# Kernel tuning notes

Measured on AMD Instinct MI355X. Metric: run time of the kernel, lower is better.

## Reference

```python
import jax, jax.numpy as jnp
import numpy as np

B, C, H, W, T_PREV, HEADS, KSIZE = 16, 512, 28, 28, 15, 16, 5


def setup_inputs() -> dict:
    key = jax.random.key(0)
    ks = jax.random.split(key, 6)
    return {
        "x": jax.random.normal(ks[0], (B, C, H, W), jnp.float32),
        "prev_K": jax.random.normal(ks[1], (B, T_PREV, C), jnp.float32),
        "prev_V": jax.random.normal(ks[2], (B, T_PREV, C, H, W), jnp.float32) * 0.1,
        "wq": jax.random.normal(ks[3], (1, 1, KSIZE), jnp.float32) * 0.3,
        "wk": jax.random.normal(ks[4], (1, 1, KSIZE), jnp.float32) * 0.3,
        "wv": jax.random.normal(ks[5], (C, 1, 3, 3), jnp.float32) * 0.2,
    }


def _conv1d_same(y, ker):
    # y: [b,1,c], ker: [1,1,k]; SAME padding = (k-1)//2 on each side for odd k
    p = (ker.shape[-1] - 1) // 2
    return jax.lax.conv_general_dilated(
        y, ker, (1,), [(p, p)], dimension_numbers=("NCH", "OIH", "NCH"))


def _forward(x, prev_K, prev_V, wq, wk, wv):
    b, c, h, w = x.shape
    g = HEADS
    d = c // g
    norm = 1.0 / jnp.sqrt(jnp.asarray(d, x.dtype))
    # ECA-style channel attention: global avg pool -> conv1d over channels
    y = jnp.mean(x, axis=(2, 3))[:, None, :]            # [b,1,c]
    Q = _conv1d_same(y, wq)[:, 0, :]                    # [b,c]
    k = _conv1d_same(y, wk)                             # [b,1,c]
    # depthwise 3x3 conv for V
    v = jax.lax.conv_general_dilated(
        x, wv, (1, 1), [(1, 1), (1, 1)],
        dimension_numbers=("NCHW", "OIHW", "NCHW"), feature_group_count=c)
    # grow recurrent caches
    K = jnp.concatenate([prev_K, k], axis=1)            # [b,t,c]
    V = jnp.concatenate([prev_V, v[:, None]], axis=1)   # [b,t,c,h,w]
    t = K.shape[1]
    # grouped decode attention: single query step vs t cached steps
    Qg = Q.reshape(b, g, d)                             # [b,g,d]
    Kg = K.reshape(b, t, g, d)                          # [b,t,g,d]
    atten = jnp.einsum("bgd,btgd->bgt", Qg, Kg) * norm  # [b,g,t]
    atten = jax.nn.softmax(atten, axis=-1)
    Vg = V.reshape(b, t, g, d, h, w)                    # [b,t,g,d,h,w]
    out = jnp.einsum("bgt,btgdhw->bgdhw", atten, Vg).reshape(b, c, h, w)
    return out, K, V


def reference(x, prev_K, prev_V, wq, wk, wv):
    return _forward(x, prev_K, prev_V, wq, wk, wv)
```

## Files before the change

### kernel.cpp

```cpp
#include <hip/hip_runtime.h>
#include <hip/hip_bf16.h>

#define B_ 16
#define C_ 512
#define H_ 28
#define W_ 28
#define TPREV 15
#define TT 16
#define HEADS_ 16
#define DHEAD 32
#define HW 784
#define HW4 196
#define CH4 (C_ * HW4)
#define NORM 0.17677669529663687f

typedef float f32x4 __attribute__((ext_vector_type(4)));

#define POOL_BLOCKS (B_ * C_)
#define KCOPY_QUADS (B_ * TPREV * C_ / 4)
#define KCOPY_BLOCKS (KCOPY_QUADS / 64)

__global__ __launch_bounds__(64) void pool_copy_kernel(const float* __restrict__ x,
                                                       const float* __restrict__ prevK,
                                                       float* __restrict__ y,
                                                       float* __restrict__ Kout) {
    const int lane = threadIdx.x;
    if (blockIdx.x < POOL_BLOCKS) {
        const int bc = blockIdx.x;
        const f32x4* __restrict__ xr = (const f32x4*)(x + (size_t)bc * HW);
        float s = 0.0f;
        for (int i = lane; i < HW4; i += 64) {
            f32x4 v = xr[i];
            s += v.x + v.y + v.z + v.w;
        }
        #pragma unroll
        for (int off = 32; off > 0; off >>= 1) s += __shfl_down(s, off);
        if (lane == 0) y[bc] = s * (1.0f / (float)HW);
    } else {
        const int j = (blockIdx.x - POOL_BLOCKS) * 64 + lane;
        const f32x4* __restrict__ src = (const f32x4*)prevK;
        f32x4* __restrict__ dst = (f32x4*)Kout;
        const int b = j / (TPREV * C_ / 4);
        dst[j + b * (C_ / 4)] = src[j];
    }
}

__global__ __launch_bounds__(256) void fuse_kernel(const float* __restrict__ x,
                                                   const float* __restrict__ prevV,
                                                   const float* __restrict__ prevK,
                                                   const float* __restrict__ y,
                                                   const float* __restrict__ wq,
                                                   const float* __restrict__ wk,
                                                   const float* __restrict__ wv,
                                                   float* __restrict__ out,
                                                   float* __restrict__ Kout,
                                                   float* __restrict__ Vout) {
    const int tid = threadIdx.x;
    const int blk0 = blockIdx.x * 256;
    __shared__ float att_s[3][TT];

    const int bc_lo = blk0 / HW4;
    const int bc_hi = (blk0 + 255) / HW4;

    if (tid < 96) {
        const int half = tid >> 5;
        const int d    = tid & 31;
        const int bcx  = bc_lo + half;
        if (bcx <= bc_hi) {
            const int bb = bcx >> 9;
            const int gg = (bcx & (C_ - 1)) >> 5;
            const int cc = gg * DHEAD + d;

            float Qc = 0.0f, kc = 0.0f;
            #pragma unroll
            for (int j = 0; j < 5; ++j) {
                const int cj = cc - 2 + j;
                const float yv = (cj >= 0 && cj < C_) ? y[bb * C_ + cj] : 0.0f;
                Qc = fmaf(yv, wq[j], Qc);
                kc = fmaf(yv, wk[j], kc);
            }

            float pl[TT];
            #pragma unroll
            for (int t = 0; t < TPREV; ++t)
                pl[t] = Qc * prevK[((size_t)bb * TPREV + t) * C_ + cc];
            pl[TPREV] = Qc * kc;

            #pragma unroll
            for (int m = 1; m <= 16; m <<= 1) {
                #pragma unroll
                for (int t = 0; t < TT; ++t)
                    pl[t] += __shfl_xor(pl[t], m);
            }

            float mx = -1e30f;
            #pragma unroll
            for (int t = 0; t < TT; ++t) mx = fmaxf(mx, pl[t] * NORM);
            float sum = 0.0f;
            #pragma unroll
            for (int t = 0; t < TT; ++t) sum += __expf(pl[t] * NORM - mx);
            if (d < TT)
                att_s[half][d] = __expf(pl[d] * NORM - mx) / sum;

            const int qk = (bb * C_ + cc) * HW4;
            if (qk >= blk0 && qk < blk0 + 256)
                Kout[((size_t)bb * TT + TPREV) * C_ + cc] = kc;
        }
    }
    __syncthreads();

    const int i  = blk0 + tid;
    const int p4 = i % HW4;
    const int bc = i / HW4;
    const int c  = bc & (C_ - 1);
    const int b  = bc >> 9;
    const int h_ = bc - bc_lo;

    f32x4* __restrict__ Vo = (f32x4*)Vout;
    const f32x4* __restrict__ Pv = (const f32x4*)prevV;
    const size_t pvq = ((size_t)b * TPREV * C_ + c) * HW4 + p4;
    const size_t voq = ((size_t)b * TT    * C_ + c) * HW4 + p4;

    f32x4 pv[TPREV];
    #pragma unroll
    for (int t = 0; t < TPREV; ++t)
        pv[t] = __builtin_nontemporal_load(&Pv[pvq + (size_t)t * CH4]);

    const float* __restrict__ xbc = x + (size_t)bc * HW;
    const int p  = p4 * 4;
    const int h  = p / W_;
    const int w0 = p % W_;
    float r[3][6];
    #pragma unroll
    for (int ry = 0; ry < 3; ++ry) {
        const int hh = h - 1 + ry;
        if (hh < 0 || hh >= H_) {
            #pragma unroll
            for (int j = 0; j < 6; ++j) r[ry][j] = 0.0f;
        } else {
            const float* row = xbc + hh * W_;
            f32x4 mid = *(const f32x4*)(row + w0);
            r[ry][1] = mid.x; r[ry][2] = mid.y; r[ry][3] = mid.z; r[ry][4] = mid.w;
            r[ry][0] = (w0 > 0)      ? row[w0 - 1] : 0.0f;
            r[ry][5] = (w0 + 4 < W_) ? row[w0 + 4] : 0.0f;
        }
    }
    float wv9[9];
    #pragma unroll
    for (int k = 0; k < 9; ++k) wv9[k] = wv[c * 9 + k];

    f32x4 v4;
    #pragma unroll
    for (int j = 0; j < 4; ++j) {
        float s = 0.0f;
        #pragma unroll
        for (int ky = 0; ky < 3; ++ky)
            #pragma unroll
            for (int kx = 0; kx < 3; ++kx)
                s = fmaf(r[ky][j + kx], wv9[ky * 3 + kx], s);
        v4[j] = s;
    }

    f32x4 acc;
    {
        const float a = att_s[h_][TPREV];
        __builtin_nontemporal_store(v4, &Vo[voq + (size_t)TPREV * CH4]);
        acc = v4 * a;
    }

    #pragma unroll
    for (int t = 0; t < TPREV; ++t) {
        __builtin_nontemporal_store(pv[t], &Vo[voq + (size_t)t * CH4]);
        const float a = att_s[h_][t];
        acc.x = fmaf(a, pv[t].x, acc.x);
        acc.y = fmaf(a, pv[t].y, acc.y);
        acc.z = fmaf(a, pv[t].z, acc.z);
        acc.w = fmaf(a, pv[t].w, acc.w);
    }
    __builtin_nontemporal_store(acc, &((f32x4*)out)[(size_t)bc * HW4 + p4]);
}

extern "C" void kernel_launch(void* const* d_in, const int* in_sizes, int n_in,
                              void* d_out, int out_size, void* d_ws, size_t ws_size,
                              hipStream_t stream) {
    const float* x     = (const float*)d_in[0];
    const float* prevK = (const float*)d_in[1];
    const float* prevV = (const float*)d_in[2];
    const float* wq    = (const float*)d_in[3];
    const float* wk    = (const float*)d_in[4];
    const float* wv    = (const float*)d_in[5];

    float* out  = (float*)d_out;
    float* Kout = out + (size_t)B_ * C_ * HW;
    float* Vout = Kout + (size_t)B_ * TT * C_;

    float* y_ws = (float*)d_ws;

    pool_copy_kernel<<<POOL_BLOCKS + KCOPY_BLOCKS, 64, 0, stream>>>(x, prevK, y_ws, Kout);

    const int totalq = B_ * C_ * HW4;
    fuse_kernel<<<totalq / 256, 256, 0, stream>>>(x, prevV, prevK, y_ws, wq, wk, wv,
                                                  out, Kout, Vout);
}
```

Baseline: 159.9 us.

## Merge pooling and attention kernels into one cooperative persistent kernel with grid sync

Replaces the two-kernel sequence (pool/K-copy, then fused attention) with a single cooperative kernel. It does the pooling and K copy with grid-stride loops, synchronizes the whole grid, then runs the attention/V work over persistent blocks. The aim is to remove the second launch and the gap between kernels. In exchange it adds a grid-wide barrier, caps the grid at 896 blocks, and runs an occupancy query on the host every call.

```diff
diff --git a/kernel.cpp b/kernel.cpp
--- a/kernel.cpp
+++ b/kernel.cpp
@@ -1,5 +1,7 @@
 #include <hip/hip_runtime.h>
-#include <hip/hip_bf16.h>
+#include <hip/hip_cooperative_groups.h>
+
+namespace cg = cooperative_groups;
 
 #define B_ 16
 #define C_ 512
@@ -14,170 +16,177 @@
 #define CH4 (C_ * HW4)
 #define NORM 0.17677669529663687f
 
+#define POOL_UNITS (B_ * C_)
+#define KCOPY_QUADS (B_ * TPREV * C_ / 4)
+#define NUNITS (B_ * C_ * HW4 / 256)
+
 typedef float f32x4 __attribute__((ext_vector_type(4)));
 
-#define POOL_BLOCKS (B_ * C_)
-#define KCOPY_QUADS (B_ * TPREV * C_ / 4)
-#define KCOPY_BLOCKS (KCOPY_QUADS / 64)
-
-__global__ __launch_bounds__(64) void pool_copy_kernel(const float* __restrict__ x,
-                                                       const float* __restrict__ prevK,
-                                                       float* __restrict__ y,
-                                                       float* __restrict__ Kout) {
-    const int lane = threadIdx.x;
-    if (blockIdx.x < POOL_BLOCKS) {
-        const int bc = blockIdx.x;
-        const f32x4* __restrict__ xr = (const f32x4*)(x + (size_t)bc * HW);
-        float s = 0.0f;
-        for (int i = lane; i < HW4; i += 64) {
-            f32x4 v = xr[i];
-            s += v.x + v.y + v.z + v.w;
-        }
-        #pragma unroll
-        for (int off = 32; off > 0; off >>= 1) s += __shfl_down(s, off);
-        if (lane == 0) y[bc] = s * (1.0f / (float)HW);
-    } else {
-        const int j = (blockIdx.x - POOL_BLOCKS) * 64 + lane;
-        const f32x4* __restrict__ src = (const f32x4*)prevK;
-        f32x4* __restrict__ dst = (f32x4*)Kout;
-        const int b = j / (TPREV * C_ / 4);
-        dst[j + b * (C_ / 4)] = src[j];
-    }
-}
-
-__global__ __launch_bounds__(256) void fuse_kernel(const float* __restrict__ x,
+__global__ __launch_bounds__(256) void mega_kernel(const float* __restrict__ x,
+                                                   const float* __restrict__ prevK,
                                                    const float* __restrict__ prevV,
-                                                   const float* __restrict__ prevK,
-                                                   const float* __restrict__ y,
                                                    const float* __restrict__ wq,
                                                    const float* __restrict__ wk,
                                                    const float* __restrict__ wv,
                                                    float* __restrict__ out,
                                                    float* __restrict__ Kout,
-                                                   float* __restrict__ Vout) {
+                                                   float* __restrict__ Vout,
+                                                   float* __restrict__ y) {
     const int tid = threadIdx.x;
-    const int blk0 = blockIdx.x * 256;
+    const int nb  = gridDim.x;
     __shared__ float att_s[3][TT];
 
-    const int bc_lo = blk0 / HW4;
-    const int bc_hi = (blk0 + 255) / HW4;
-
-    if (tid < 96) {
-        const int half = tid >> 5;
-        const int d    = tid & 31;
-        const int bcx  = bc_lo + half;
-        if (bcx <= bc_hi) {
-            const int bb = bcx >> 9;
-            const int gg = (bcx & (C_ - 1)) >> 5;
-            const int cc = gg * DHEAD + d;
-
-            float Qc = 0.0f, kc = 0.0f;
+    {
+        const int lane   = tid & 63;
+        const int nwaves = nb * 4;
+        for (int u = blockIdx.x * 4 + (tid >> 6); u < POOL_UNITS; u += nwaves) {
+            const f32x4* __restrict__ xr = (const f32x4*)(x + (size_t)u * HW);
+            float s = 0.0f;
+            for (int i = lane; i < HW4; i += 64) {
+                f32x4 v = xr[i];
+                s += v.x + v.y + v.z + v.w;
+            }
             #pragma unroll
-            for (int j = 0; j < 5; ++j) {
-                const int cj = cc - 2 + j;
-                const float yv = (cj >= 0 && cj < C_) ? y[bb * C_ + cj] : 0.0f;
-                Qc = fmaf(yv, wq[j], Qc);
-                kc = fmaf(yv, wk[j], kc);
+            for (int off = 32; off > 0; off >>= 1) s += __shfl_down(s, off);
+            if (lane == 0) y[u] = s * (1.0f / (float)HW);
+        }
+    }
+    {
+        const int nthr = nb * 256;
+        const f32x4* __restrict__ src = (const f32x4*)prevK;
+        f32x4* __restrict__ dst = (f32x4*)Kout;
+        for (int j = blockIdx.x * 256 + tid; j < KCOPY_QUADS; j += nthr) {
+            const int b = j / (TPREV * C_ / 4);
+            dst[j + b * (C_ / 4)] = src[j];
+        }
+    }
+
+    cg::this_grid().sync();
+
+    for (int u = blockIdx.x; u < NUNITS; u += nb) {
+        const int blk0  = u * 256;
+        const int bc_lo = blk0 / HW4;
+        const int bc_hi = (blk0 + 255) / HW4;
+
+        __syncthreads();
+
+        if (tid < 96) {
+            const int half = tid >> 5;
+            const int d    = tid & 31;
+            const int bcx  = bc_lo + half;
+            if (bcx <= bc_hi) {
+                const int bb = bcx >> 9;
+                const int gg = (bcx & (C_ - 1)) >> 5;
+                const int cc = gg * DHEAD + d;
+
+                float Qc = 0.0f, kc = 0.0f;
+                #pragma unroll
+                for (int j = 0; j < 5; ++j) {
+                    const int cj = cc - 2 + j;
+                    const float yv = (cj >= 0 && cj < C_) ? y[bb * C_ + cj] : 0.0f;
+                    Qc = fmaf(yv, wq[j], Qc);
+                    kc = fmaf(yv, wk[j], kc);
+                }
+
+                float pl[TT];
+                #pragma unroll
+                for (int t = 0; t < TPREV; ++t)
+                    pl[t] = Qc * prevK[((size_t)bb * TPREV + t) * C_ + cc];
+                pl[TPREV] = Qc * kc;
+
+                #pragma unroll
+                for (int m = 1; m <= 16; m <<= 1) {
+                    #pragma unroll
+                    for (int t = 0; t < TT; ++t)
+                        pl[t] += __shfl_xor(pl[t], m);
+                }
+
+                float mx = -1e30f;
+                #pragma unroll
+                for (int t = 0; t < TT; ++t) mx = fmaxf(mx, pl[t] * NORM);
+                float sum = 0.0f;
+                #pragma unroll
+                for (int t = 0; t < TT; ++t) sum += __expf(pl[t] * NORM - mx);
+                if (d < TT)
+                    att_s[half][d] = __expf(pl[d] * NORM - mx) / sum;
+
+                const int qk = (bb * C_ + cc) * HW4;
+                if (qk >= blk0 && qk < blk0 + 256)
+                    Kout[((size_t)bb * TT + TPREV) * C_ + cc] = kc;
             }
-
-            float pl[TT];
+        }
+        __syncthreads();
+
+        const int i  = blk0 + tid;
+        const int p4 = i % HW4;
+        const int bc = i / HW4;
+        const int c  = bc & (C_ - 1);
+        const int b  = bc >> 9;
+        const int h_ = bc - bc_lo;
+
+        f32x4* __restrict__ Vo = (f32x4*)Vout;
+        const f32x4* __restrict__ Pv = (const f32x4*)prevV;
+        const size_t pvq = ((size_t)b * TPREV * C_ + c) * HW4 + p4;
+        const size_t voq = ((size_t)b * TT    * C_ + c) * HW4 + p4;
+
+        f32x4 pv[TPREV];
+        #pragma unroll
+        for (int t = 0; t < TPREV; ++t)
+            pv[t] = __builtin_nontemporal_load(&Pv[pvq + (size_t)t * CH4]);
+
+        const float* __restrict__ xbc = x + (size_t)bc * HW;
+        const int p  = p4 * 4;
+        const int h  = p / W_;
+        const int w0 = p % W_;
+        float r[3][6];
+        #pragma unroll
+        for (int ry = 0; ry < 3; ++ry) {
+            const int hh = h - 1 + ry;
+            if (hh < 0 || hh >= H_) {
+                #pragma unroll
+                for (int j = 0; j < 6; ++j) r[ry][j] = 0.0f;
+            } else {
+                const float* row = xbc + hh * W_;
+                f32x4 mid = *(const f32x4*)(row + w0);
+                r[ry][1] = mid.x; r[ry][2] = mid.y; r[ry][3] = mid.z; r[ry][4] = mid.w;
+                r[ry][0] = (w0 > 0)      ? row[w0 - 1] : 0.0f;
+                r[ry][5] = (w0 + 4 < W_) ? row[w0 + 4] : 0.0f;
+            }
+        }
+        float wv9[9];
+        #pragma unroll
+        for (int k = 0; k < 9; ++k) wv9[k] = wv[c * 9 + k];
+
+        f32x4 v4;
+        #pragma unroll
+        for (int j = 0; j < 4; ++j) {
+            float s = 0.0f;
             #pragma unroll
-            for (int t = 0; t < TPREV; ++t)
-                pl[t] = Qc * prevK[((size_t)bb * TPREV + t) * C_ + cc];
-            pl[TPREV] = Qc * kc;
-
-            #pragma unroll
-            for (int m = 1; m <= 16; m <<= 1) {
-                #pragma unroll
-                for (int t = 0; t < TT; ++t)
-                    pl[t] += __shfl_xor(pl[t], m);
-            }
-
-            float mx = -1e30f;
-            #pragma unroll
-            for (int t = 0; t < TT; ++t) mx = fmaxf(mx, pl[t] * NORM);
-            float sum = 0.0f;
-            #pragma unroll
-            for (int t = 0; t < TT; ++t) sum += __expf(pl[t] * NORM - mx);
-            if (d < TT)
-                att_s[half][d] = __expf(pl[d] * NORM - mx) / sum;
-
-            const int qk = (bb * C_ + cc) * HW4;
-            if (qk >= blk0 && qk < blk0 + 256)
-                Kout[((size_t)bb * TT + TPREV) * C_ + cc] = kc;
-        }
+            for (int ky = 0; ky < 3; ++ky)
+                #pragma unroll
+                for (int kx = 0; kx < 3; ++kx)
+                    s = fmaf(r[ky][j + kx], wv9[ky * 3 + kx], s);
+            v4[j] = s;
+        }
+
+        f32x4 acc;
+        {
+            const float a = att_s[h_][TPREV];
+            __builtin_nontemporal_store(v4, &Vo[voq + (size_t)TPREV * CH4]);
+            acc = v4 * a;
+        }
+
+        #pragma unroll
+        for (int t = 0; t < TPREV; ++t) {
+            __builtin_nontemporal_store(pv[t], &Vo[voq + (size_t)t * CH4]);
+            const float a = att_s[h_][t];
+            acc.x = fmaf(a, pv[t].x, acc.x);
+            acc.y = fmaf(a, pv[t].y, acc.y);
+            acc.z = fmaf(a, pv[t].z, acc.z);
+            acc.w = fmaf(a, pv[t].w, acc.w);
+        }
+        __builtin_nontemporal_store(acc, &((f32x4*)out)[(size_t)bc * HW4 + p4]);
     }
-    __syncthreads();
-
-    const int i  = blk0 + tid;
-    const int p4 = i % HW4;
-    const int bc = i / HW4;
-    const int c  = bc & (C_ - 1);
-    const int b  = bc >> 9;
-    const int h_ = bc - bc_lo;
-
-    f32x4* __restrict__ Vo = (f32x4*)Vout;
-    const f32x4* __restrict__ Pv = (const f32x4*)prevV;
-    const size_t pvq = ((size_t)b * TPREV * C_ + c) * HW4 + p4;
-    const size_t voq = ((size_t)b * TT    * C_ + c) * HW4 + p4;
-
-    f32x4 pv[TPREV];
-    #pragma unroll
-    for (int t = 0; t < TPREV; ++t)
-        pv[t] = __builtin_nontemporal_load(&Pv[pvq + (size_t)t * CH4]);
-
-    const float* __restrict__ xbc = x + (size_t)bc * HW;
-    const int p  = p4 * 4;
-    const int h  = p / W_;
-    const int w0 = p % W_;
-    float r[3][6];
-    #pragma unroll
-    for (int ry = 0; ry < 3; ++ry) {
-        const int hh = h - 1 + ry;
-        if (hh < 0 || hh >= H_) {
-            #pragma unroll
-            for (int j = 0; j < 6; ++j) r[ry][j] = 0.0f;
-        } else {
-            const float* row = xbc + hh * W_;
-            f32x4 mid = *(const f32x4*)(row + w0);
-            r[ry][1] = mid.x; r[ry][2] = mid.y; r[ry][3] = mid.z; r[ry][4] = mid.w;
-            r[ry][0] = (w0 > 0)      ? row[w0 - 1] : 0.0f;
-            r[ry][5] = (w0 + 4 < W_) ? row[w0 + 4] : 0.0f;
-        }
-    }
-    float wv9[9];
-    #pragma unroll
-    for (int k = 0; k < 9; ++k) wv9[k] = wv[c * 9 + k];
-
-    f32x4 v4;
-    #pragma unroll
-    for (int j = 0; j < 4; ++j) {
-        float s = 0.0f;
-        #pragma unroll
-        for (int ky = 0; ky < 3; ++ky)
-            #pragma unroll
-            for (int kx = 0; kx < 3; ++kx)
-                s = fmaf(r[ky][j + kx], wv9[ky * 3 + kx], s);
-        v4[j] = s;
-    }
-
-    f32x4 acc;
-    {
-        const float a = att_s[h_][TPREV];
-        __builtin_nontemporal_store(v4, &Vo[voq + (size_t)TPREV * CH4]);
-        acc = v4 * a;
-    }
-
-    #pragma unroll
-    for (int t = 0; t < TPREV; ++t) {
-        __builtin_nontemporal_store(pv[t], &Vo[voq + (size_t)t * CH4]);
-        const float a = att_s[h_][t];
-        acc.x = fmaf(a, pv[t].x, acc.x);
-        acc.y = fmaf(a, pv[t].y, acc.y);
-        acc.z = fmaf(a, pv[t].z, acc.z);
-        acc.w = fmaf(a, pv[t].w, acc.w);
-    }
-    __builtin_nontemporal_store(acc, &((f32x4*)out)[(size_t)bc * HW4 + p4]);
 }
 
 extern "C" void kernel_launch(void* const* d_in, const int* in_sizes, int n_in,
@@ -196,9 +205,14 @@
 
     float* y_ws = (float*)d_ws;
 
-    pool_copy_kernel<<<POOL_BLOCKS + KCOPY_BLOCKS, 64, 0, stream>>>(x, prevK, y_ws, Kout);
-
-    const int totalq = B_ * C_ * HW4;
-    fuse_kernel<<<totalq / 256, 256, 0, stream>>>(x, prevV, prevK, y_ws, wq, wk, wv,
-                                                  out, Kout, Vout);
+    int occ = 0;
+    (void)hipOccupancyMaxActiveBlocksPerMultiprocessor(&occ, mega_kernel, 256, 0);
+    if (occ < 1) occ = 1;
+    int grid = occ * 256;
+    if (grid > 896) grid = 896;
+
+    void* args[] = {(void*)&x, (void*)&prevK, (void*)&prevV, (void*)&wq, (void*)&wk,
+                    (void*)&wv, (void*)&out, (void*)&Kout, (void*)&Vout, (void*)&y_ws};
+    (void)hipLaunchCooperativeKernel((void*)mega_kernel, dim3(grid), dim3(256),
+                                     args, 0, stream);
 }
```

Measured after the change: 208.0 us. +30.1%, slower.
